# Performance work log

Measured on AMD Instinct MI355X. Metric: run time of the kernel, lower is better.

The kernel has to match this reference:

```python
import jax, jax.numpy as jnp
import numpy as np

TAU = 0.05
EPS = 1e-12


def _l2_normalize(x):
    # F.normalize(p=2): x / max(||x||, eps)
    n = jnp.sqrt(jnp.sum(x * x, axis=-1, keepdims=True))
    return x / jnp.maximum(n, EPS)


def _masked_lse(sim, mask):
    # logsumexp over axis -1 restricted to mask; rows with empty mask are
    # masked out downstream (has_pos), so we guard the log to stay finite.
    neg_inf = jnp.finfo(sim.dtype).min
    mx = jnp.max(jnp.where(mask, sim, neg_inf), axis=-1)
    mx_safe = jnp.where(mx > neg_inf / 2, mx, 0.0)
    s = jnp.sum(jnp.where(mask, jnp.exp(sim - mx_safe[:, None]), 0.0), axis=-1)
    return mx_safe + jnp.log(jnp.where(s > 0, s, 1.0))


def setup_inputs() -> dict:
    key = jax.random.key(0)
    k1, k2, k3, k4 = jax.random.split(key, 4)
    B, S, D = 64, 128, 256
    return {
        "logits": jax.random.normal(k1, (B, S, D), dtype=jnp.float32),
        "labels": jax.random.normal(k2, (B, S, D), dtype=jnp.float32),
        "pad_mask": jax.random.randint(k3, (B, S), 0, 2, dtype=jnp.int32),
        "ad_idxs": jax.random.randint(k4, (B, S), 0, 500, dtype=jnp.int32),
    }


def reference(logits, labels, pad_mask, ad_idxs):
    B, S, D = logits.shape
    q = _l2_normalize(logits.reshape(B * S, D))
    k = _l2_normalize(labels.reshape(B * S, D))
    valid = pad_mask.reshape(B * S).astype(bool)
    ad = ad_idxs.reshape(B * S)

    sim = jnp.einsum("nd,md->nm", q, k) / TAU          # [N, N]
    pair_valid = valid[None, :] & valid[:, None]
    pos_mask = (ad[None, :] == ad[:, None]) & pair_valid

    pos_lse = _masked_lse(sim, pos_mask)
    all_lse = _masked_lse(sim, pair_valid)
    has_pos = jnp.any(pos_mask, axis=-1)

    loss_per_row = -(pos_lse - all_lse)
    # mean over rows with at least one positive (== loss_per_row[has_pos].mean())
    cnt = jnp.sum(has_pos.astype(sim.dtype))
    loss = jnp.sum(jnp.where(has_pos, loss_per_row, 0.0)) / jnp.maximum(cnt, 1.0)
    return loss
```

## Files before the change

### kernel.cpp

```cpp
#include <hip/hip_runtime.h>
#include <hip/hip_bf16.h>
#include <hip/hip_fp8.h>
#include <math.h>

typedef float f32x4 __attribute__((ext_vector_type(4)));
typedef int   i32x4 __attribute__((ext_vector_type(4)));
typedef int   v8i   __attribute__((ext_vector_type(8)));

constexpr int Nn = 8192;
constexpr int Dd = 256;
constexpr float LOG2E     = 1.4426950408889634f;
constexpr float SIM_SCALE = 20.0f * LOG2E;
constexpr float SIM_BIAS  = -20.0f * LOG2E;
constexpr int   SCALE1    = 0x7F7F7F7F;

typedef __attribute__((address_space(1))) const unsigned int gu32;
typedef __attribute__((address_space(3))) unsigned int lu32;
__device__ __forceinline__ void gload16(const unsigned char* g, unsigned char* l) {
  __builtin_amdgcn_global_load_lds((gu32*)(uintptr_t)g, (lu32*)(uintptr_t)l, 16, 0, 0);
}

__global__ __launch_bounds__(256) void prep_kernel(const float* __restrict__ logits,
                                                   const float* __restrict__ labels,
                                                   const int* __restrict__ pad,
                                                   unsigned char* __restrict__ qb,
                                                   unsigned char* __restrict__ kb,
                                                   float* __restrict__ cbias,
                                                   float* __restrict__ g_all,
                                                   float* __restrict__ g_pos) {
  const int j = blockIdx.x * 256 + threadIdx.x;
  if (j < Nn) {
    cbias[j] = pad[j] ? SIM_BIAS : -1e30f;
    g_all[j] = 0.0f;
    g_pos[j] = 0.0f;
  }

  const int gw   = (blockIdx.x * 256 + threadIdx.x) >> 6;
  const int lane = threadIdx.x & 63;
  const float* src;
  unsigned char* dst;
  int row;
  if (gw < Nn) { src = logits; dst = qb; row = gw; }
  else         { src = labels; dst = kb; row = gw - Nn; }

  const float4 v = *reinterpret_cast<const float4*>(src + (size_t)row * Dd + lane * 4);
  float ss = v.x * v.x + v.y * v.y + v.z * v.z + v.w * v.w;
#pragma unroll
  for (int m = 32; m >= 1; m >>= 1) ss += __shfl_xor(ss, m);
  const float scale = 1.0f / fmaxf(sqrtf(ss), 1e-12f);

  const __hip_fp8_e4m3 e0(v.x * scale);
  const __hip_fp8_e4m3 e1(v.y * scale);
  const __hip_fp8_e4m3 e2(v.z * scale);
  const __hip_fp8_e4m3 e3(v.w * scale);
  const unsigned int packed = (unsigned int)e0.__x |
                              ((unsigned int)e1.__x << 8) |
                              ((unsigned int)e2.__x << 16) |
                              ((unsigned int)e3.__x << 24);
  reinterpret_cast<unsigned int*>(dst + (size_t)row * Dd)[lane] = packed;
}

__global__ __launch_bounds__(256) void gemm_lse_kernel(const unsigned char* __restrict__ qb,
                                                       const unsigned char* __restrict__ kb,
                                                       const float* __restrict__ cbias,
                                                       const int* __restrict__ ad,
                                                       float* __restrict__ g_all,
                                                       float* __restrict__ g_pos) {
  __shared__ unsigned char smem[49152];
  unsigned char* As = smem;
  float* redA = reinterpret_cast<float*>(smem);
  float* redP = reinterpret_cast<float*>(smem) + 2048;

  const int tid  = threadIdx.x;
  const int lane = tid & 63;
  const int w    = tid >> 6;
  const int wrow = (w >> 1) * 64;
  const int wcol = (w & 1) * 64;
  const int lq   = lane & 15;
  const int qd   = lane >> 4;
  const int rowBase = blockIdx.x * 256;
  const int colBase = blockIdx.y * 128;

  const int srl = lane >> 3;
  const int cg  = (lane & 7) ^ srl;
  const unsigned char* gA0 = qb + (size_t)(rowBase + w * 32 + srl) * Dd + cg * 16;
  const unsigned char* gB0 = kb + (size_t)(colBase + w * 32 + srl) * Dd + cg * 16;

#pragma unroll
  for (int kkb = 0; kkb < 2; ++kkb)
#pragma unroll
    for (int i = 0; i < 4; ++i)
      gload16(gB0 + (size_t)i * 8 * Dd + kkb * 128,
              &smem[16384 + kkb * 16384 + (w * 32 + i * 8) * 128]);

  float colB[4];
  int colAd[4];
#pragma unroll
  for (int nt = 0; nt < 4; ++nt) {
    const int col = colBase + wcol + nt * 16 + lq;
    colB[nt]  = cbias[col];
    colAd[nt] = ad[col];
  }

  for (int pass = 0; pass < 2; ++pass) {
    const int rowOff = pass * 128;

    f32x4 c[4][4];
#pragma unroll
    for (int mt = 0; mt < 4; ++mt)
#pragma unroll
      for (int nt = 0; nt < 4; ++nt)
        c[mt][nt] = (f32x4){0.f, 0.f, 0.f, 0.f};

    for (int kk = 0; kk < 2; ++kk) {
      const int kOff = kk * 128;
      __syncthreads();
#pragma unroll
      for (int i = 0; i < 4; ++i)
        gload16(gA0 + (size_t)(rowOff + i * 8) * Dd + kOff,
                &As[(w * 32 + i * 8) * 128]);
      __syncthreads();

      const int g0 = qd << 1;
      v8i af[4];
#pragma unroll
      for (int mt = 0; mt < 4; ++mt) {
        const int r = wrow + mt * 16 + lq;
        const i32x4 lo = *reinterpret_cast<const i32x4*>(&As[r * 128 + ((g0 ^ (r & 7)) << 4)]);
        const i32x4 hi = *reinterpret_cast<const i32x4*>(&As[r * 128 + (((g0 + 1) ^ (r & 7)) << 4)]);
        af[mt] = (v8i){lo.x, lo.y, lo.z, lo.w, hi.x, hi.y, hi.z, hi.w};
      }
      const unsigned char* BsH = &smem[16384 + kk * 16384];
#pragma unroll
      for (int nt = 0; nt < 4; ++nt) {
        const int r = wcol + nt * 16 + lq;
        const i32x4 lo = *reinterpret_cast<const i32x4*>(&BsH[r * 128 + ((g0 ^ (r & 7)) << 4)]);
        const i32x4 hi = *reinterpret_cast<const i32x4*>(&BsH[r * 128 + (((g0 + 1) ^ (r & 7)) << 4)]);
        const v8i bfq = (v8i){lo.x, lo.y, lo.z, lo.w, hi.x, hi.y, hi.z, hi.w};
#pragma unroll
        for (int mt = 0; mt < 4; ++mt)
          c[mt][nt] = __builtin_amdgcn_mfma_scale_f32_16x16x128_f8f6f4(
              af[mt], bfq, c[mt][nt], 0, 0, 0, SCALE1, 0, SCALE1);
      }
    }

    __syncthreads();

#pragma unroll
    for (int mt = 0; mt < 4; ++mt) {
#pragma unroll
      for (int r = 0; r < 4; ++r) {
        const int row   = wrow + mt * 16 + qd * 4 + r;
        const int rowAd = ad[rowBase + rowOff + row];
        float a = 0.f, p = 0.f;
#pragma unroll
        for (int nt = 0; nt < 4; ++nt) {
          const float e = __builtin_amdgcn_exp2f(fmaf(c[mt][nt][r], SIM_SCALE, colB[nt]));
          a += e;
          p += (colAd[nt] == rowAd) ? e : 0.f;
        }
        a += __shfl_xor(a, 8);
        p += __shfl_xor(p, 8);
        if (lq < 8) {
          const int idx = (w & 1) * 8 + lq;
          const int g   = idx >> 2;
          const int gi  = idx & 3;
          const int off = row * 16 + ((g ^ (row & 3)) << 2) + gi;
          redA[off] = a;
          redP[off] = p;
        }
      }
    }
    __syncthreads();

    if (tid < 128) {
      const int row = tid;
      float a = 0.f, p = 0.f;
#pragma unroll
      for (int gg = 0; gg < 4; ++gg) {
        const int off = row * 16 + ((gg ^ (row & 3)) << 2);
        const f32x4 va = *reinterpret_cast<const f32x4*>(&redA[off]);
        const f32x4 vp = *reinterpret_cast<const f32x4*>(&redP[off]);
        a += (va[0] + va[1]) + (va[2] + va[3]);
        p += (vp[0] + vp[1]) + (vp[2] + vp[3]);
      }
      atomicAdd(&g_all[rowBase + rowOff + row], a);
      atomicAdd(&g_pos[rowBase + rowOff + row], p);
    }
  }
}

__global__ __launch_bounds__(1024) void reduce_kernel(const float* __restrict__ g_all,
                                                      const float* __restrict__ g_pos,
                                                      const int* __restrict__ pad,
                                                      float* __restrict__ out) {
  __shared__ float sS[16], sC[16];
  const int t = threadIdx.x;
  float s = 0.f, c = 0.f;
  const float4* ga4 = (const float4*)g_all;
  const float4* gp4 = (const float4*)g_pos;
  const int4*   pd4 = (const int4*)pad;
  for (int i = t; i < Nn / 4; i += 1024) {
    const float4 ga = ga4[i];
    const float4 gp = gp4[i];
    const int4   pd = pd4[i];
    if (pd.x) { s += __logf(ga.x) - __logf(gp.x); c += 1.f; }
    if (pd.y) { s += __logf(ga.y) - __logf(gp.y); c += 1.f; }
    if (pd.z) { s += __logf(ga.z) - __logf(gp.z); c += 1.f; }
    if (pd.w) { s += __logf(ga.w) - __logf(gp.w); c += 1.f; }
  }
#pragma unroll
  for (int m = 32; m >= 1; m >>= 1) {
    s += __shfl_xor(s, m);
    c += __shfl_xor(c, m);
  }
  if ((t & 63) == 0) { sS[t >> 6] = s; sC[t >> 6] = c; }
  __syncthreads();
  if (t == 0) {
    float S = 0.f, C = 0.f;
#pragma unroll
    for (int i = 0; i < 16; ++i) { S += sS[i]; C += sC[i]; }
    out[0] = S / fmaxf(C, 1.0f);
  }
}

extern "C" void kernel_launch(void* const* d_in, const int* in_sizes, int n_in,
                              void* d_out, int out_size, void* d_ws, size_t ws_size,
                              hipStream_t stream) {
  const float* logits = (const float*)d_in[0];
  const float* labels = (const float*)d_in[1];
  const int*   pad    = (const int*)d_in[2];
  const int*   ad     = (const int*)d_in[3];

  char* ws = (char*)d_ws;
  unsigned char* qb = (unsigned char*)(ws);
  unsigned char* kb = (unsigned char*)(ws + 2097152);
  float*  cb   = (float*)(ws + 4194304);
  float*  gAll = (float*)(ws + 4227072);
  float*  gPos = (float*)(ws + 4259840);
  float*  out  = (float*)d_out;

  prep_kernel<<<4096, 256, 0, stream>>>(logits, labels, pad, qb, kb, cb, gAll, gPos);
  gemm_lse_kernel<<<dim3(32, 64), 256, 0, stream>>>(qb, kb, cb, ad, gAll, gPos);
  reduce_kernel<<<1, 1024, 0, stream>>>(gAll, gPos, pad, out);
}
```

Before: 118.4 us.

## Keep Q tile resident and stream K tiles with double buffering per block

Each block now loads a 128-row Q tile once into LDS and iterates over 1024 columns of K in 8 sub-tiles. The next K half-tile is prefetched into a double buffer while MFMAs run on the current one. Per-row exp sums are kept in registers across column tiles and reduced with shuffles, so the LDS reduction stage goes away and far fewer global atomics are issued. The grid shrinks from 2048 to 512 blocks, which lowers parallelism, and the larger LDS footprint plus launch_bounds(256,2) may limit occupancy.

```diff
diff --git a/kernel.cpp b/kernel.cpp
--- a/kernel.cpp
+++ b/kernel.cpp
@@ -60,26 +60,23 @@
   reinterpret_cast<unsigned int*>(dst + (size_t)row * Dd)[lane] = packed;
 }
 
-__global__ __launch_bounds__(256) void gemm_lse_kernel(const unsigned char* __restrict__ qb,
-                                                       const unsigned char* __restrict__ kb,
-                                                       const float* __restrict__ cbias,
-                                                       const int* __restrict__ ad,
-                                                       float* __restrict__ g_all,
-                                                       float* __restrict__ g_pos) {
-  __shared__ unsigned char smem[49152];
-  unsigned char* As = smem;
-  float* redA = reinterpret_cast<float*>(smem);
-  float* redP = reinterpret_cast<float*>(smem) + 2048;
+__global__ __launch_bounds__(256, 2) void gemm_lse_kernel(const unsigned char* __restrict__ qb,
+                                                          const unsigned char* __restrict__ kb,
+                                                          const float* __restrict__ cbias,
+                                                          const int* __restrict__ ad,
+                                                          float* __restrict__ g_all,
+                                                          float* __restrict__ g_pos) {
+  __shared__ unsigned char smem[65536];
 
   const int tid  = threadIdx.x;
   const int lane = tid & 63;
   const int w    = tid >> 6;
   const int wrow = (w >> 1) * 64;
-  const int wcol = (w & 1) * 64;
+  const int wcolL = (w & 1) * 64;
   const int lq   = lane & 15;
   const int qd   = lane >> 4;
-  const int rowBase = blockIdx.x * 256;
-  const int colBase = blockIdx.y * 128;
+  const int rowBase = blockIdx.x * 128;
+  const int colBase = blockIdx.y * 1024;
 
   const int srl = lane >> 3;
   const int cg  = (lane & 7) ^ srl;
@@ -87,105 +84,125 @@
   const unsigned char* gB0 = kb + (size_t)(colBase + w * 32 + srl) * Dd + cg * 16;
 
 #pragma unroll
-  for (int kkb = 0; kkb < 2; ++kkb)
+  for (int kk = 0; kk < 2; ++kk)
 #pragma unroll
     for (int i = 0; i < 4; ++i)
-      gload16(gB0 + (size_t)i * 8 * Dd + kkb * 128,
-              &smem[16384 + kkb * 16384 + (w * 32 + i * 8) * 128]);
+      gload16(gA0 + (size_t)i * 8 * Dd + kk * 128,
+              &smem[kk * 16384 + (w * 32 + i * 8) * 128]);
+#pragma unroll
+  for (int i = 0; i < 4; ++i)
+    gload16(gB0 + (size_t)i * 8 * Dd, &smem[32768 + (w * 32 + i * 8) * 128]);
+
+  int rowAd[4][4];
+#pragma unroll
+  for (int mt = 0; mt < 4; ++mt)
+#pragma unroll
+    for (int r = 0; r < 4; ++r)
+      rowAd[mt][r] = ad[rowBase + wrow + mt * 16 + qd * 4 + r];
+
+  float apA[4][4], apP[4][4];
+  f32x4 c[4][4];
+#pragma unroll
+  for (int mt = 0; mt < 4; ++mt)
+#pragma unroll
+    for (int r = 0; r < 4; ++r) {
+      apA[mt][r] = 0.f;
+      apP[mt][r] = 0.f;
+      c[mt][r] = (f32x4){0.f, 0.f, 0.f, 0.f};
+    }
 
   float colB[4];
   int colAd[4];
-#pragma unroll
-  for (int nt = 0; nt < 4; ++nt) {
-    const int col = colBase + wcol + nt * 16 + lq;
-    colB[nt]  = cbias[col];
-    colAd[nt] = ad[col];
-  }
-
-  for (int pass = 0; pass < 2; ++pass) {
-    const int rowOff = pass * 128;
-
-    f32x4 c[4][4];
-#pragma unroll
-    for (int mt = 0; mt < 4; ++mt)
-#pragma unroll
-      for (int nt = 0; nt < 4; ++nt)
-        c[mt][nt] = (f32x4){0.f, 0.f, 0.f, 0.f};
-
-    for (int kk = 0; kk < 2; ++kk) {
-      const int kOff = kk * 128;
-      __syncthreads();
+
+  __syncthreads();
+
+  for (int t = 0; t < 16; ++t) {
+    const int kk = t & 1;
+
+    if (t + 1 < 16) {
+      const int tn = t + 1;
+      const unsigned char* g = gB0 + (size_t)((tn >> 1) * 128) * Dd + (tn & 1) * 128;
+      unsigned char* dB = &smem[32768 + (tn & 1) * 16384 + (w * 32) * 128];
 #pragma unroll
       for (int i = 0; i < 4; ++i)
-        gload16(gA0 + (size_t)(rowOff + i * 8) * Dd + kOff,
-                &As[(w * 32 + i * 8) * 128]);
-      __syncthreads();
-
-      const int g0 = qd << 1;
-      v8i af[4];
+        gload16(g + (size_t)i * 8 * Dd, dB + i * 8 * 128);
+    }
+
+    if (kk == 0) {
+      const int ct = t >> 1;
+#pragma unroll
+      for (int nt = 0; nt < 4; ++nt) {
+        const int col = colBase + ct * 128 + wcolL + nt * 16 + lq;
+        colB[nt]  = cbias[col];
+        colAd[nt] = ad[col];
+      }
+    }
+
+    const int g0 = qd << 1;
+    const unsigned char* Ah = &smem[kk * 16384];
+    const unsigned char* Bh = &smem[32768 + (t & 1) * 16384];
+
+    v8i af[4];
+#pragma unroll
+    for (int mt = 0; mt < 4; ++mt) {
+      const int r = wrow + mt * 16 + lq;
+      const i32x4 lo = *reinterpret_cast<const i32x4*>(&Ah[r * 128 + ((g0 ^ (r & 7)) << 4)]);
+      const i32x4 hi = *reinterpret_cast<const i32x4*>(&Ah[r * 128 + (((g0 + 1) ^ (r & 7)) << 4)]);
+      af[mt] = (v8i){lo.x, lo.y, lo.z, lo.w, hi.x, hi.y, hi.z, hi.w};
+    }
+#pragma unroll
+    for (int nt = 0; nt < 4; ++nt) {
+      const int r = wcolL + nt * 16 + lq;
+      const i32x4 lo = *reinterpret_cast<const i32x4*>(&Bh[r * 128 + ((g0 ^ (r & 7)) << 4)]);
+      const i32x4 hi = *reinterpret_cast<const i32x4*>(&Bh[r * 128 + (((g0 + 1) ^ (r & 7)) << 4)]);
+      const v8i bfq = (v8i){lo.x, lo.y, lo.z, lo.w, hi.x, hi.y, hi.z, hi.w};
+#pragma unroll
+      for (int mt = 0; mt < 4; ++mt)
+        c[mt][nt] = __builtin_amdgcn_mfma_scale_f32_16x16x128_f8f6f4(
+            af[mt], bfq, c[mt][nt], 0, 0, 0, SCALE1, 0, SCALE1);
+    }
+
+    if (kk == 1) {
 #pragma unroll
       for (int mt = 0; mt < 4; ++mt) {
-        const int r = wrow + mt * 16 + lq;
-        const i32x4 lo = *reinterpret_cast<const i32x4*>(&As[r * 128 + ((g0 ^ (r & 7)) << 4)]);
-        const i32x4 hi = *reinterpret_cast<const i32x4*>(&As[r * 128 + (((g0 + 1) ^ (r & 7)) << 4)]);
-        af[mt] = (v8i){lo.x, lo.y, lo.z, lo.w, hi.x, hi.y, hi.z, hi.w};
-      }
-      const unsigned char* BsH = &smem[16384 + kk * 16384];
-#pragma unroll
-      for (int nt = 0; nt < 4; ++nt) {
-        const int r = wcol + nt * 16 + lq;
-        const i32x4 lo = *reinterpret_cast<const i32x4*>(&BsH[r * 128 + ((g0 ^ (r & 7)) << 4)]);
-        const i32x4 hi = *reinterpret_cast<const i32x4*>(&BsH[r * 128 + (((g0 + 1) ^ (r & 7)) << 4)]);
-        const v8i bfq = (v8i){lo.x, lo.y, lo.z, lo.w, hi.x, hi.y, hi.z, hi.w};
-#pragma unroll
-        for (int mt = 0; mt < 4; ++mt)
-          c[mt][nt] = __builtin_amdgcn_mfma_scale_f32_16x16x128_f8f6f4(
-              af[mt], bfq, c[mt][nt], 0, 0, 0, SCALE1, 0, SCALE1);
-      }
+#pragma unroll
+        for (int r = 0; r < 4; ++r) {
+          float a = 0.f, p = 0.f;
+#pragma unroll
+          for (int nt = 0; nt < 4; ++nt) {
+            const float e = __builtin_amdgcn_exp2f(fmaf(c[mt][nt][r], SIM_SCALE, colB[nt]));
+            a += e;
+            p += (colAd[nt] == rowAd[mt][r]) ? e : 0.f;
+          }
+          apA[mt][r] += a;
+          apP[mt][r] += p;
+        }
+      }
+#pragma unroll
+      for (int mt = 0; mt < 4; ++mt)
+#pragma unroll
+        for (int nt = 0; nt < 4; ++nt)
+          c[mt][nt] = (f32x4){0.f, 0.f, 0.f, 0.f};
     }
 
     __syncthreads();
-
-#pragma unroll
-    for (int mt = 0; mt < 4; ++mt) {
-#pragma unroll
-      for (int r = 0; r < 4; ++r) {
-        const int row   = wrow + mt * 16 + qd * 4 + r;
-        const int rowAd = ad[rowBase + rowOff + row];
-        float a = 0.f, p = 0.f;
-#pragma unroll
-        for (int nt = 0; nt < 4; ++nt) {
-          const float e = __builtin_amdgcn_exp2f(fmaf(c[mt][nt][r], SIM_SCALE, colB[nt]));
-          a += e;
-          p += (colAd[nt] == rowAd) ? e : 0.f;
-        }
-        a += __shfl_xor(a, 8);
-        p += __shfl_xor(p, 8);
-        if (lq < 8) {
-          const int idx = (w & 1) * 8 + lq;
-          const int g   = idx >> 2;
-          const int gi  = idx & 3;
-          const int off = row * 16 + ((g ^ (row & 3)) << 2) + gi;
-          redA[off] = a;
-          redP[off] = p;
-        }
-      }
-    }
-    __syncthreads();
-
-    if (tid < 128) {
-      const int row = tid;
-      float a = 0.f, p = 0.f;
-#pragma unroll
-      for (int gg = 0; gg < 4; ++gg) {
-        const int off = row * 16 + ((gg ^ (row & 3)) << 2);
-        const f32x4 va = *reinterpret_cast<const f32x4*>(&redA[off]);
-        const f32x4 vp = *reinterpret_cast<const f32x4*>(&redP[off]);
-        a += (va[0] + va[1]) + (va[2] + va[3]);
-        p += (vp[0] + vp[1]) + (vp[2] + vp[3]);
-      }
-      atomicAdd(&g_all[rowBase + rowOff + row], a);
-      atomicAdd(&g_pos[rowBase + rowOff + row], p);
+  }
+
+#pragma unroll
+  for (int mt = 0; mt < 4; ++mt) {
+#pragma unroll
+    for (int r = 0; r < 4; ++r) {
+      float a = apA[mt][r], p = apP[mt][r];
+#pragma unroll
+      for (int m = 1; m < 16; m <<= 1) {
+        a += __shfl_xor(a, m);
+        p += __shfl_xor(p, m);
+      }
+      if (lq == 0) {
+        const int row = rowBase + wrow + mt * 16 + qd * 4 + r;
+        atomicAdd(&g_all[row], a);
+        atomicAdd(&g_pos[row], p);
+      }
     }
   }
 }
@@ -241,6 +258,6 @@
   float*  out  = (float*)d_out;
 
   prep_kernel<<<4096, 256, 0, stream>>>(logits, labels, pad, qb, kb, cb, gAll, gPos);
-  gemm_lse_kernel<<<dim3(32, 64), 256, 0, stream>>>(qb, kb, cb, ad, gAll, gPos);
+  gemm_lse_kernel<<<dim3(64, 8), 256, 0, stream>>>(qb, kb, cb, ad, gAll, gPos);
   reduce_kernel<<<1, 1024, 0, stream>>>(gAll, gPos, pad, out);
 }
```

After: 104.2 us. 1.14x faster.
